# Kernel optimization log

Measured on AMD Instinct MI355X. Metric: run time of the kernel, lower is better.

The kernel has to match this reference:

```python
import jax, jax.numpy as jnp
import numpy as np

B, L, D = 8, 2048, 64


def setup_inputs() -> dict:
    key = jax.random.key(0)
    kq, kk, kv = jax.random.split(key, 3)
    query = jax.random.normal(kq, (B, L, D), dtype=jnp.float32)
    key_t = jax.random.normal(kk, (B, L, D), dtype=jnp.float32)
    value = jax.random.normal(kv, (B, L, D), dtype=jnp.float32)
    return {"query": query, "key": key_t, "value": value}


def reference(query, key, value):
    d = query.shape[-1]
    # e = Q K^T / sqrt(d_k)   -> [B, Lq, Lk]
    scale = 1.0 / np.sqrt(float(d)).astype(np.float32)
    e = jnp.einsum("bqd,bkd->bqk", query, key) * scale
    # stable softmax over keys (matches exp(e - max)/sum in source)
    attention = jax.nn.softmax(e, axis=-1)
    # v = A V   -> [B, Lq, Dv]
    return jnp.einsum("bqk,bkd->bqd", attention, value)
```

## Files before the change

### kernel.cpp

```cpp
#include <hip/hip_runtime.h>


#define B_ 8
#define L_ 2048
#define D_ 64

typedef _Float16 half8_t __attribute__((ext_vector_type(8)));
typedef _Float16 half4_t __attribute__((ext_vector_type(4)));
typedef float f32x4 __attribute__((ext_vector_type(4)));

#define SCALE_LOG2E 0.1803368801111244f

__global__ __launch_bounds__(512, 2) void attn_fused(
    const float* __restrict__ Q, const float* __restrict__ K,
    const float* __restrict__ V, float* __restrict__ O)
{
    __shared__ __align__(16) _Float16 FR[16384];

    const int t    = threadIdx.x;
    const int wave = t >> 6;
    const int lane = t & 63;
    const int quad = lane >> 4;
    const int l15  = lane & 15;
    const int qg   = wave & 3;
    const int kg   = wave >> 2;

    const int b   = blockIdx.x & 7;
    const int qbi = blockIdx.x >> 3;
    const int qb  = qbi * 64;

    const size_t boff = (size_t)b * L_ * D_;

    const int skg = t >> 8;
    const int kj  = t & 255;
    const int kp    = kj >> 6, kjl = kj & 63;
    const int kquad = kjl >> 4, kl15 = kjl & 15;
    const int ks_ = kp >> 1, kc = kp & 1;
    const int ksrc0 = (ks_ * 16 + kl15) * D_ + kc * 32 + kquad * 8;
    const int kldst = skg * 4096 + kp * 512 + kjl * 8;

    int vsrc0[2], vldst[2];
    #pragma unroll
    for (int i = 0; i < 2; ++i) {
        const int j  = (t & 255) * 2 + i;
        const int p  = j >> 6, jl = j & 63;
        const int vq = jl >> 4, vl = jl & 15;
        const int d  = p >> 1, vks = p & 1;
        vsrc0[i] = (vks * 16 + vq * 4) * D_ + d * 16 + vl;
        vldst[i] = skg * 4096 + 2048 + p * 256 + jl * 4;
    }
    const int tile0 = skg * 32;

    half8_t bq[2];
    {
        const float* qp = Q + boff + (size_t)(qb + qg * 16 + l15) * D_ + quad * 8;
        #pragma unroll
        for (int c = 0; c < 2; ++c) {
            const float4 f0 = *(const float4*)(qp + c * 32);
            const float4 f1 = *(const float4*)(qp + c * 32 + 4);
            bq[c][0] = (_Float16)(f0.x * SCALE_LOG2E);
            bq[c][1] = (_Float16)(f0.y * SCALE_LOG2E);
            bq[c][2] = (_Float16)(f0.z * SCALE_LOG2E);
            bq[c][3] = (_Float16)(f0.w * SCALE_LOG2E);
            bq[c][4] = (_Float16)(f1.x * SCALE_LOG2E);
            bq[c][5] = (_Float16)(f1.y * SCALE_LOG2E);
            bq[c][6] = (_Float16)(f1.z * SCALE_LOG2E);
            bq[c][7] = (_Float16)(f1.w * SCALE_LOG2E);
        }
    }

    f32x4 ofr[4];
    #pragma unroll
    for (int d = 0; d < 4; ++d) ofr[d] = (f32x4){0.f, 0.f, 0.f, 0.f};
    float lacc = 0.f;

    float4 kf0, kf1;
    float  vf[2][4];

#define GLOAD(TT)                                                              \
    {                                                                          \
        const float* kpp = K + boff + (size_t)(tile0 + (TT)) * 32 * D_ + ksrc0;\
        kf0 = *(const float4*)kpp;                                             \
        kf1 = *(const float4*)(kpp + 4);                                       \
        _Pragma("unroll") for (int i = 0; i < 2; ++i) {                        \
            const float* vpp =                                                 \
                V + boff + (size_t)(tile0 + (TT)) * 32 * D_ + vsrc0[i];        \
            vf[i][0] = vpp[0];      vf[i][1] = vpp[D_];                        \
            vf[i][2] = vpp[2 * D_]; vf[i][3] = vpp[3 * D_];                    \
        }                                                                      \
    }

#define SWRITE(BUF)                                                            \
    {                                                                          \
        half8_t w;                                                             \
        w[0] = (_Float16)kf0.x; w[1] = (_Float16)kf0.y;                        \
        w[2] = (_Float16)kf0.z; w[3] = (_Float16)kf0.w;                        \
        w[4] = (_Float16)kf1.x; w[5] = (_Float16)kf1.y;                        \
        w[6] = (_Float16)kf1.z; w[7] = (_Float16)kf1.w;                        \
        *(half8_t*)&FR[(BUF) * 8192 + kldst] = w;                              \
        _Pragma("unroll") for (int i = 0; i < 2; ++i) {                        \
            half4_t a;                                                         \
            a[0] = (_Float16)vf[i][0]; a[1] = (_Float16)vf[i][1];              \
            a[2] = (_Float16)vf[i][2]; a[3] = (_Float16)vf[i][3];              \
            *(half4_t*)&FR[(BUF) * 8192 + vldst[i]] = a;                       \
        }                                                                      \
    }

    GLOAD(0);
    SWRITE(0);
    GLOAD(1);
    __syncthreads();

    const _Float16* Kb = &FR[kg * 4096];
    const _Float16* Vb = Kb + 2048;

    for (int tt = 0; tt < 32; ++tt) {
        const int cb = (tt & 1) * 8192;
        if (tt < 31) {
            SWRITE((tt & 1) ^ 1);
            if (tt < 30) GLOAD(tt + 2);
        }
        half8_t bk[2][2];
        #pragma unroll
        for (int s = 0; s < 2; ++s)
            #pragma unroll
            for (int c = 0; c < 2; ++c)
                bk[s][c] = *(const half8_t*)&Kb[cb + (s * 2 + c) * 512 + lane * 8];
        half4_t av[4][2];
        #pragma unroll
        for (int d = 0; d < 4; ++d)
            #pragma unroll
            for (int ks = 0; ks < 2; ++ks)
                av[d][ks] = *(const half4_t*)&Vb[cb + (d * 2 + ks) * 256 + lane * 4];
        #pragma unroll
        for (int ks = 0; ks < 2; ++ks) {
            f32x4 acc = (f32x4){0.f, 0.f, 0.f, 0.f};
            acc = __builtin_amdgcn_mfma_f32_16x16x32_f16(bk[ks][0], bq[0], acc, 0, 0, 0);
            acc = __builtin_amdgcn_mfma_f32_16x16x32_f16(bk[ks][1], bq[1], acc, 0, 0, 0);
            const float p0 = __builtin_exp2f(acc[0]);
            const float p1 = __builtin_exp2f(acc[1]);
            const float p2 = __builtin_exp2f(acc[2]);
            const float p3 = __builtin_exp2f(acc[3]);
            lacc += (p0 + p1) + (p2 + p3);
            half4_t pv;
            pv[0] = (_Float16)p0; pv[1] = (_Float16)p1;
            pv[2] = (_Float16)p2; pv[3] = (_Float16)p3;
            #pragma unroll
            for (int d = 0; d < 4; ++d)
                ofr[d] = __builtin_amdgcn_mfma_f32_16x16x16f16(av[d][ks], pv, ofr[d], 0, 0, 0);
        }
        __syncthreads();
    }

    float lsum = lacc;
    lsum += __shfl_xor(lsum, 16, 64);
    lsum += __shfl_xor(lsum, 32, 64);

    float* red = (float*)&FR[0];
    if (kg == 1) {
        float* dst = red + (qg * 64 + lane) * 17;
        #pragma unroll
        for (int d = 0; d < 4; ++d)
            #pragma unroll
            for (int r = 0; r < 4; ++r) dst[d * 4 + r] = ofr[d][r];
        dst[16] = lsum;
    }
    __syncthreads();
    if (kg == 0) {
        const float* src = red + (qg * 64 + lane) * 17;
        const float inv = 1.0f / (lsum + src[16]);
        #pragma unroll
        for (int d = 0; d < 4; ++d) {
            float4 o;
            o.x = (ofr[d][0] + src[d * 4 + 0]) * inv;
            o.y = (ofr[d][1] + src[d * 4 + 1]) * inv;
            o.z = (ofr[d][2] + src[d * 4 + 2]) * inv;
            o.w = (ofr[d][3] + src[d * 4 + 3]) * inv;
            *(float4*)&O[boff + (size_t)(qb + qg * 16 + l15) * D_ + d * 16 + quad * 4] = o;
        }
    }
}

extern "C" void kernel_launch(void* const* d_in, const int* in_sizes, int n_in,
                              void* d_out, int out_size, void* d_ws, size_t ws_size,
                              hipStream_t stream) {
    const float* Q = (const float*)d_in[0];
    const float* K = (const float*)d_in[1];
    const float* V = (const float*)d_in[2];
    float* O = (float*)d_out;
    (void)d_ws; (void)ws_size;
    attn_fused<<<256, 512, 0, stream>>>(Q, K, V, O);
}
```

Before: 92.34 us.

## Split key sequence across 8 wave groups with 1024-thread blocks and cross-wave reduction

```diff
diff --git a/kernel.cpp b/kernel.cpp
--- a/kernel.cpp
+++ b/kernel.cpp
@@ -11,98 +11,108 @@
 
 #define SCALE_LOG2E 0.1803368801111244f
 
-__global__ __launch_bounds__(512, 2) void attn_fused(
+__global__ __launch_bounds__(1024) void attn_fused2(
     const float* __restrict__ Q, const float* __restrict__ K,
     const float* __restrict__ V, float* __restrict__ O)
 {
-    __shared__ __align__(16) _Float16 FR[16384];
+    __shared__ __align__(16) _Float16 FR[65536];
 
     const int t    = threadIdx.x;
     const int wave = t >> 6;
     const int lane = t & 63;
     const int quad = lane >> 4;
     const int l15  = lane & 15;
-    const int qg   = wave & 3;
-    const int kg   = wave >> 2;
-
-    const int b   = blockIdx.x & 7;
-    const int qbi = blockIdx.x >> 3;
-    const int qb  = qbi * 64;
+    const int kg   = wave >> 1;
+    const int qg   = wave & 1;
+
+    const int b  = blockIdx.x & 7;
+    const int qc = blockIdx.x >> 3;
+    const int q0 = qc * 64 + qg * 32;
 
     const size_t boff = (size_t)b * L_ * D_;
 
-    const int skg = t >> 8;
-    const int kj  = t & 255;
-    const int kp    = kj >> 6, kjl = kj & 63;
-    const int kquad = kjl >> 4, kl15 = kjl & 15;
-    const int ks_ = kp >> 1, kc = kp & 1;
-    const int ksrc0 = (ks_ * 16 + kl15) * D_ + kc * 32 + kquad * 8;
-    const int kldst = skg * 4096 + kp * 512 + kjl * 8;
-
-    int vsrc0[2], vldst[2];
-    #pragma unroll
-    for (int i = 0; i < 2; ++i) {
-        const int j  = (t & 255) * 2 + i;
-        const int p  = j >> 6, jl = j & 63;
-        const int vq = jl >> 4, vl = jl & 15;
-        const int d  = p >> 1, vks = p & 1;
-        vsrc0[i] = (vks * 16 + vq * 4) * D_ + d * 16 + vl;
-        vldst[i] = skg * 4096 + 2048 + p * 256 + jl * 4;
-    }
-    const int tile0 = skg * 32;
-
-    half8_t bq[2];
-    {
-        const float* qp = Q + boff + (size_t)(qb + qg * 16 + l15) * D_ + quad * 8;
+    int ksrc[2], kdst[2];
+    #pragma unroll
+    for (int j = 0; j < 2; ++j) {
+        const int gk = j * 1024 + t;
+        const int kgs = gk >> 8, kj = gk & 255;
+        const int p = kj >> 6, jl = kj & 63;
+        const int jq = jl >> 4, jl15 = jl & 15;
+        const int s = p >> 1, c = p & 1;
+        ksrc[j] = (kgs * 256 + s * 16 + jl15) * D_ + c * 32 + jq * 8;
+        kdst[j] = kgs * 4096 + p * 512 + jl * 8;
+    }
+    int vsrc[4], vdst[4];
+    #pragma unroll
+    for (int j = 0; j < 4; ++j) {
+        const int gv = j * 1024 + t;
+        const int kgs = gv >> 9, vj = gv & 511;
+        const int p = vj >> 6, jl = vj & 63;
+        const int jq = jl >> 4, jl15 = jl & 15;
+        const int d = p >> 1, ks = p & 1;
+        vsrc[j] = (kgs * 256 + ks * 16 + jq * 4) * D_ + d * 16 + jl15;
+        vdst[j] = kgs * 4096 + 2048 + d * 512 + jl * 8 + ks * 4;
+    }
+
+    half8_t bq[2][2];
+    #pragma unroll
+    for (int qs = 0; qs < 2; ++qs) {
+        const float* qp = Q + boff + (size_t)(q0 + qs * 16 + l15) * D_ + quad * 8;
         #pragma unroll
         for (int c = 0; c < 2; ++c) {
             const float4 f0 = *(const float4*)(qp + c * 32);
             const float4 f1 = *(const float4*)(qp + c * 32 + 4);
-            bq[c][0] = (_Float16)(f0.x * SCALE_LOG2E);
-            bq[c][1] = (_Float16)(f0.y * SCALE_LOG2E);
-            bq[c][2] = (_Float16)(f0.z * SCALE_LOG2E);
-            bq[c][3] = (_Float16)(f0.w * SCALE_LOG2E);
-            bq[c][4] = (_Float16)(f1.x * SCALE_LOG2E);
-            bq[c][5] = (_Float16)(f1.y * SCALE_LOG2E);
-            bq[c][6] = (_Float16)(f1.z * SCALE_LOG2E);
-            bq[c][7] = (_Float16)(f1.w * SCALE_LOG2E);
-        }
-    }
-
-    f32x4 ofr[4];
-    #pragma unroll
-    for (int d = 0; d < 4; ++d) ofr[d] = (f32x4){0.f, 0.f, 0.f, 0.f};
-    float lacc = 0.f;
-
-    float4 kf0, kf1;
-    float  vf[2][4];
+            bq[qs][c][0] = (_Float16)(f0.x * SCALE_LOG2E);
+            bq[qs][c][1] = (_Float16)(f0.y * SCALE_LOG2E);
+            bq[qs][c][2] = (_Float16)(f0.z * SCALE_LOG2E);
+            bq[qs][c][3] = (_Float16)(f0.w * SCALE_LOG2E);
+            bq[qs][c][4] = (_Float16)(f1.x * SCALE_LOG2E);
+            bq[qs][c][5] = (_Float16)(f1.y * SCALE_LOG2E);
+            bq[qs][c][6] = (_Float16)(f1.z * SCALE_LOG2E);
+            bq[qs][c][7] = (_Float16)(f1.w * SCALE_LOG2E);
+        }
+    }
+
+    f32x4 ofr[2][4];
+    #pragma unroll
+    for (int qs = 0; qs < 2; ++qs)
+        #pragma unroll
+        for (int d = 0; d < 4; ++d)
+            ofr[qs][d] = (f32x4){0.f, 0.f, 0.f, 0.f};
+    float lacc[2] = {0.f, 0.f};
+
+    float4 kf[2][2];
+    float  vf[4][4];
 
 #define GLOAD(TT)                                                              \
     {                                                                          \
-        const float* kpp = K + boff + (size_t)(tile0 + (TT)) * 32 * D_ + ksrc0;\
-        kf0 = *(const float4*)kpp;                                             \
-        kf1 = *(const float4*)(kpp + 4);                                       \
-        _Pragma("unroll") for (int i = 0; i < 2; ++i) {                        \
-            const float* vpp =                                                 \
-                V + boff + (size_t)(tile0 + (TT)) * 32 * D_ + vsrc0[i];        \
-            vf[i][0] = vpp[0];      vf[i][1] = vpp[D_];                        \
-            vf[i][2] = vpp[2 * D_]; vf[i][3] = vpp[3 * D_];                    \
+        _Pragma("unroll") for (int j = 0; j < 2; ++j) {                        \
+            const float* kp = K + boff + (size_t)(TT) * 32 * D_ + ksrc[j];     \
+            kf[j][0] = *(const float4*)kp;                                     \
+            kf[j][1] = *(const float4*)(kp + 4);                               \
+        }                                                                      \
+        _Pragma("unroll") for (int j = 0; j < 4; ++j) {                        \
+            const float* vp = V + boff + (size_t)(TT) * 32 * D_ + vsrc[j];     \
+            vf[j][0] = vp[0];      vf[j][1] = vp[D_];                          \
+            vf[j][2] = vp[2 * D_]; vf[j][3] = vp[3 * D_];                      \
         }                                                                      \
     }
 
 #define SWRITE(BUF)                                                            \
     {                                                                          \
-        half8_t w;                                                             \
-        w[0] = (_Float16)kf0.x; w[1] = (_Float16)kf0.y;                        \
-        w[2] = (_Float16)kf0.z; w[3] = (_Float16)kf0.w;                        \
-        w[4] = (_Float16)kf1.x; w[5] = (_Float16)kf1.y;                        \
-        w[6] = (_Float16)kf1.z; w[7] = (_Float16)kf1.w;                        \
-        *(half8_t*)&FR[(BUF) * 8192 + kldst] = w;                              \
-        _Pragma("unroll") for (int i = 0; i < 2; ++i) {                        \
+        _Pragma("unroll") for (int j = 0; j < 2; ++j) {                        \
+            half8_t w;                                                         \
+            w[0] = (_Float16)kf[j][0].x; w[1] = (_Float16)kf[j][0].y;          \
+            w[2] = (_Float16)kf[j][0].z; w[3] = (_Float16)kf[j][0].w;          \
+            w[4] = (_Float16)kf[j][1].x; w[5] = (_Float16)kf[j][1].y;          \
+            w[6] = (_Float16)kf[j][1].z; w[7] = (_Float16)kf[j][1].w;          \
+            *(half8_t*)&FR[(BUF) * 32768 + kdst[j]] = w;                       \
+        }                                                                      \
+        _Pragma("unroll") for (int j = 0; j < 4; ++j) {                        \
             half4_t a;                                                         \
-            a[0] = (_Float16)vf[i][0]; a[1] = (_Float16)vf[i][1];              \
-            a[2] = (_Float16)vf[i][2]; a[3] = (_Float16)vf[i][3];              \
-            *(half4_t*)&FR[(BUF) * 8192 + vldst[i]] = a;                       \
+            a[0] = (_Float16)vf[j][0]; a[1] = (_Float16)vf[j][1];              \
+            a[2] = (_Float16)vf[j][2]; a[3] = (_Float16)vf[j][3];              \
+            *(half4_t*)&FR[(BUF) * 32768 + vdst[j]] = a;                       \
         }                                                                      \
     }
 
@@ -111,72 +121,98 @@
     GLOAD(1);
     __syncthreads();
 
-    const _Float16* Kb = &FR[kg * 4096];
-    const _Float16* Vb = Kb + 2048;
-
-    for (int tt = 0; tt < 32; ++tt) {
-        const int cb = (tt & 1) * 8192;
-        if (tt < 31) {
-            SWRITE((tt & 1) ^ 1);
-            if (tt < 30) GLOAD(tt + 2);
-        }
+    for (int i = 0; i < 8; ++i) {
+        const int cb = (i & 1) * 32768;
+        if (i < 7) {
+            SWRITE((i & 1) ^ 1);
+            if (i < 6) GLOAD(i + 2);
+        }
+        const _Float16* Kt = &FR[cb + kg * 4096];
+        const _Float16* Vt = Kt + 2048;
         half8_t bk[2][2];
         #pragma unroll
         for (int s = 0; s < 2; ++s)
             #pragma unroll
             for (int c = 0; c < 2; ++c)
-                bk[s][c] = *(const half8_t*)&Kb[cb + (s * 2 + c) * 512 + lane * 8];
-        half4_t av[4][2];
+                bk[s][c] = *(const half8_t*)&Kt[(s * 2 + c) * 512 + lane * 8];
+        half4_t pb[2][2];
+        #pragma unroll
+        for (int ks = 0; ks < 2; ++ks)
+            #pragma unroll
+            for (int qs = 0; qs < 2; ++qs) {
+                f32x4 acc = (f32x4){0.f, 0.f, 0.f, 0.f};
+                acc = __builtin_amdgcn_mfma_f32_16x16x32_f16(bk[ks][0], bq[qs][0], acc, 0, 0, 0);
+                acc = __builtin_amdgcn_mfma_f32_16x16x32_f16(bk[ks][1], bq[qs][1], acc, 0, 0, 0);
+                const float p0 = __builtin_exp2f(acc[0]);
+                const float p1 = __builtin_exp2f(acc[1]);
+                const float p2 = __builtin_exp2f(acc[2]);
+                const float p3 = __builtin_exp2f(acc[3]);
+                lacc[qs] += (p0 + p1) + (p2 + p3);
+                half4_t pw;
+                pw[0] = (_Float16)p0; pw[1] = (_Float16)p1;
+                pw[2] = (_Float16)p2; pw[3] = (_Float16)p3;
+                pb[ks][qs] = pw;
+            }
+        #pragma unroll
+        for (int d = 0; d < 4; ++d) {
+            const half8_t av8 = *(const half8_t*)&Vt[d * 512 + lane * 8];
+            const half4_t alo = __builtin_shufflevector(av8, av8, 0, 1, 2, 3);
+            const half4_t ahi = __builtin_shufflevector(av8, av8, 4, 5, 6, 7);
+            #pragma unroll
+            for (int qs = 0; qs < 2; ++qs) {
+                ofr[qs][d] = __builtin_amdgcn_mfma_f32_16x16x16f16(alo, pb[0][qs], ofr[qs][d], 0, 0, 0);
+                ofr[qs][d] = __builtin_amdgcn_mfma_f32_16x16x16f16(ahi, pb[1][qs], ofr[qs][d], 0, 0, 0);
+            }
+        }
+        __syncthreads();
+    }
+
+    float lsum[2];
+    #pragma unroll
+    for (int qs = 0; qs < 2; ++qs) {
+        float v = lacc[qs];
+        v += __shfl_xor(v, 16, 64);
+        v += __shfl_xor(v, 32, 64);
+        lsum[qs] = v;
+    }
+
+    float* RedO = (float*)&FR[0];
+    float* RedL = RedO + 17408;
+    if (quad == 0) {
+        RedL[wave * 32 + l15]      = lsum[0];
+        RedL[wave * 32 + 16 + l15] = lsum[1];
+    }
+
+    #pragma unroll
+    for (int qs = 0; qs < 2; ++qs) {
+        __syncthreads();
+        float* dst = RedO + (wave * 64 + lane) * 17;
         #pragma unroll
         for (int d = 0; d < 4; ++d)
             #pragma unroll
-            for (int ks = 0; ks < 2; ++ks)
-                av[d][ks] = *(const half4_t*)&Vb[cb + (d * 2 + ks) * 256 + lane * 4];
-        #pragma unroll
-        for (int ks = 0; ks < 2; ++ks) {
-            f32x4 acc = (f32x4){0.f, 0.f, 0.f, 0.f};
-            acc = __builtin_amdgcn_mfma_f32_16x16x32_f16(bk[ks][0], bq[0], acc, 0, 0, 0);
-            acc = __builtin_amdgcn_mfma_f32_16x16x32_f16(bk[ks][1], bq[1], acc, 0, 0, 0);
-            const float p0 = __builtin_exp2f(acc[0]);
-            const float p1 = __builtin_exp2f(acc[1]);
-            const float p2 = __builtin_exp2f(acc[2]);
-            const float p3 = __builtin_exp2f(acc[3]);
-            lacc += (p0 + p1) + (p2 + p3);
-            half4_t pv;
-            pv[0] = (_Float16)p0; pv[1] = (_Float16)p1;
-            pv[2] = (_Float16)p2; pv[3] = (_Float16)p3;
-            #pragma unroll
-            for (int d = 0; d < 4; ++d)
-                ofr[d] = __builtin_amdgcn_mfma_f32_16x16x16f16(av[d][ks], pv, ofr[d], 0, 0, 0);
-        }
+            for (int r = 0; r < 4; ++r)
+                dst[d * 4 + r] = ofr[qs][d][r];
         __syncthreads();
-    }
-
-    float lsum = lacc;
-    lsum += __shfl_xor(lsum, 16, 64);
-    lsum += __shfl_xor(lsum, 32, 64);
-
-    float* red = (float*)&FR[0];
-    if (kg == 1) {
-        float* dst = red + (qg * 64 + lane) * 17;
-        #pragma unroll
-        for (int d = 0; d < 4; ++d)
-            #pragma unroll
-            for (int r = 0; r < 4; ++r) dst[d * 4 + r] = ofr[d][r];
-        dst[16] = lsum;
-    }
-    __syncthreads();
-    if (kg == 0) {
-        const float* src = red + (qg * 64 + lane) * 17;
-        const float inv = 1.0f / (lsum + src[16]);
-        #pragma unroll
-        for (int d = 0; d < 4; ++d) {
-            float4 o;
-            o.x = (ofr[d][0] + src[d * 4 + 0]) * inv;
-            o.y = (ofr[d][1] + src[d * 4 + 1]) * inv;
-            o.z = (ofr[d][2] + src[d * 4 + 2]) * inv;
-            o.w = (ofr[d][3] + src[d * 4 + 3]) * inv;
-            *(float4*)&O[boff + (size_t)(qb + qg * 16 + l15) * D_ + d * 16 + quad * 4] = o;
+        if (wave < 8) {
+            const int rkg = wave >> 1;
+            const int rqg = wave & 1;
+            float lt = 0.f;
+            #pragma unroll
+            for (int k2 = 0; k2 < 8; ++k2)
+                lt += RedL[(k2 * 2 + rqg) * 32 + qs * 16 + l15];
+            const float inv = 1.0f / lt;
+            f32x4 osum = (f32x4){0.f, 0.f, 0.f, 0.f};
+            #pragma unroll
+            for (int k2 = 0; k2 < 8; ++k2) {
+                const float* src = RedO + ((k2 * 2 + rqg) * 64 + lane) * 17 + rkg * 4;
+                osum[0] += src[0]; osum[1] += src[1];
+                osum[2] += src[2]; osum[3] += src[3];
+            }
+            float4 outv;
+            outv.x = osum[0] * inv; outv.y = osum[1] * inv;
+            outv.z = osum[2] * inv; outv.w = osum[3] * inv;
+            *(float4*)&O[boff + (size_t)(qc * 64 + rqg * 32 + qs * 16 + l15) * D_
+                         + rkg * 16 + quad * 4] = outv;
         }
     }
 }
@@ -189,5 +225,5 @@
     const float* V = (const float*)d_in[2];
     float* O = (float*)d_out;
     (void)d_ws; (void)ws_size;
-    attn_fused<<<256, 512, 0, stream>>>(Q, K, V, O);
+    attn_fused2<<<256, 1024, 0, stream>>>(Q, K, V, O);
 }
```

After: 95.76 us. 1.04x slower.
